# Kernel optimization log

Measured on AMD Instinct MI355X. Metric: run time of the kernel, lower is better.

Reference implementation:

```python
import jax, jax.numpy as jnp
import numpy as np
import math

B, L, H, U = 4, 4096, 1024, 1024


def setup_inputs() -> dict:
    key = jax.random.key(0)
    k_in, k_wi, k_bi, k_wo, k_bo, k_u = jax.random.split(key, 6)
    inputs = jax.random.normal(k_in, (B, L, H), dtype=jnp.float32)
    # Linear layers (torch Linear: y = x @ W.T + b), scaled like torch default init
    Wi = jax.random.normal(k_wi, (U, H), dtype=jnp.float32) / math.sqrt(H)
    bi = jax.random.normal(k_bi, (U,), dtype=jnp.float32) * 0.01
    Wo = jax.random.normal(k_wo, (H, U), dtype=jnp.float32) / math.sqrt(U)
    bo = jax.random.normal(k_bo, (H,), dtype=jnp.float32) * 0.01
    # LRU-style init of nu_log / gamma_log, exactly as in the torch __init__
    r_min, r_max = 0.9, 0.999
    u = jax.random.uniform(k_u, (U,), dtype=jnp.float32)
    nu_log = jnp.log(-0.5 * jnp.log(u * (r_max ** 2 - r_min ** 2) + r_min ** 2))
    gamma_log = jnp.log(jnp.sqrt(1.0 - jnp.exp(-jnp.exp(nu_log)) ** 2))
    params_log = jnp.stack([nu_log, gamma_log])  # [2, U]
    return {"inputs": inputs, "Wi": Wi, "bi": bi, "Wo": Wo, "bo": bo,
            "params_log": params_log}


def reference(inputs, Wi, bi, Wo, bo, params_log):
    # u = i_dense(inputs): [B, L, U]
    u = jnp.einsum('blh,uh->blu', inputs, Wi) + bi
    params = jnp.exp(params_log)
    nu, gamma = params[0], params[1]  # each [U]

    log2_L = int(np.ceil(np.log2(L)))
    pad_len = 2 ** log2_L - L
    x = jnp.pad(u, ((0, 0), (0, pad_len), (0, 0))) if pad_len else u
    Lp = 2 ** log2_L

    # Log-depth doubling parallel scan: h_t = exp(-nu) * h_{t-1} + u_t
    for i in range(1, log2_L + 1):
        l = 2 ** i
        x = x.reshape(B * Lp // l, l, U)
        x1, x2 = x[:, : l // 2], x[:, l // 2:]
        pos = jnp.arange(1, l // 2 + 1, dtype=jnp.float32)  # [l/2]
        lambs = jnp.exp(-pos[:, None] * nu)                  # [l/2, U]
        x2 = x2 + lambs * x1[:, -1:]
        x = jnp.concatenate([x1, x2], axis=1).reshape(B, Lp, U)

    x = x[:, :L] * gamma
    # o_dense: [B, L, H]
    return jnp.einsum('blu,hu->blh', x, Wo) + bo
```

## Files before the change

### kernel.cpp

```cpp
#include <hip/hip_runtime.h>

#define B_DIM 4
#define L_DIM 4096
#define H_DIM 1024
#define U_DIM 1024
#define M_DIM (B_DIM * L_DIM)
#define LC 64
#define NCH (L_DIM / LC)

using f32x4  = __attribute__((ext_vector_type(4))) float;
using bf16x8 = __attribute__((ext_vector_type(8))) __bf16;
using us8    = __attribute__((ext_vector_type(8))) unsigned short;

__device__ inline unsigned short f32_to_bf16(float f) {
  unsigned int u = __float_as_uint(f);
  u += 0x7FFF + ((u >> 16) & 1);
  return (unsigned short)(u >> 16);
}
__device__ inline float bf16_to_f32(unsigned short v) {
  return __uint_as_float((unsigned int)v << 16);
}

__device__ inline void async_load16(const void* g, void* l) {
  __builtin_amdgcn_global_load_lds(
      (const __attribute__((address_space(1))) void*)g,
      (__attribute__((address_space(3))) void*)l, 16, 0, 0);
}

#define IN_ELEMS  (M_DIM * H_DIM)
#define WI_ELEMS  (U_DIM * H_DIM)
#define WO_ELEMS  (H_DIM * U_DIM)
#define CVT_TOTAL (IN_ELEMS + WI_ELEMS + WO_ELEMS)

__global__ __launch_bounds__(256) void cvt_all(
    const float* __restrict__ inp, const float* __restrict__ wi,
    const float* __restrict__ wo,
    unsigned short* __restrict__ inp_b, unsigned short* __restrict__ wi_b,
    unsigned short* __restrict__ wo_b)
{
  size_t e = ((size_t)blockIdx.x * 256 + threadIdx.x) * 8;
  if (e >= CVT_TOTAL) return;
  const float* src; unsigned short* dst; size_t off;
  if (e < IN_ELEMS)                 { src = inp; dst = inp_b; off = e; }
  else if (e < IN_ELEMS + WI_ELEMS) { src = wi;  dst = wi_b;  off = e - IN_ELEMS; }
  else                              { src = wo;  dst = wo_b;  off = e - IN_ELEMS - WI_ELEMS; }
  f32x4 a = *(const f32x4*)(src + off);
  f32x4 b = *(const f32x4*)(src + off + 4);
  us8 r;
  r[0] = f32_to_bf16(a.x); r[1] = f32_to_bf16(a.y);
  r[2] = f32_to_bf16(a.z); r[3] = f32_to_bf16(a.w);
  r[4] = f32_to_bf16(b.x); r[5] = f32_to_bf16(b.y);
  r[6] = f32_to_bf16(b.z); r[7] = f32_to_bf16(b.w);
  *(us8*)(dst + off) = r;
}

#define TM 128
#define TN 128

template <typename OUT>
__global__ __launch_bounds__(256) void gemm_bt_bias(
    const unsigned short* __restrict__ A, const unsigned short* __restrict__ Bm,
    const float* __restrict__ bias, OUT* __restrict__ C,
    int M, int N, int K)
{
  __shared__ __attribute__((aligned(16))) unsigned short sA[2][TM * 32];
  __shared__ __attribute__((aligned(16))) unsigned short sB[2][TN * 32];

  const int tid    = threadIdx.x;
  const int lane   = tid & 63;
  const int wave   = tid >> 6;
  const int wm     = wave & 1;
  const int wn     = wave >> 1;
  const int frag_m = lane & 15;
  const int frag_kb = (lane >> 4) * 16;

  const int p    = blockIdx.y * gridDim.x + blockIdx.x;
  const int xcd  = p & 7;
  const int j    = p >> 3;
  const int slab = gridDim.y >> 3;
  const int by   = xcd * slab + (j % slab);
  const int bx   = j / slab;

  const int m0 = by * TM;
  const int n0 = bx * TN;

  const char* Ab = (const char*)A;
  const char* Bb = (const char*)Bm;
  const size_t rowbytes = (size_t)K * 2;

  const int o0 = tid * 16;
  const int o1 = o0 + 4096;
  const int r0s = o0 >> 6, c0s = o0 & 63;
  const int r1s = o1 >> 6, c1s = o1 & 63;

  f32x4 acc[4][4];
  #pragma unroll
  for (int i = 0; i < 4; ++i)
    #pragma unroll
    for (int jj = 0; jj < 4; ++jj)
      acc[i][jj] = {0.f, 0.f, 0.f, 0.f};

  for (int k0 = 0; k0 < K; k0 += 64) {
    __syncthreads();
    #pragma unroll
    for (int h = 0; h < 2; ++h) {
      const size_t kb = (size_t)(k0 + h * 32) * 2;
      async_load16(Ab + (size_t)(m0 + r0s) * rowbytes + kb + c0s, (char*)sA[h] + o0);
      async_load16(Ab + (size_t)(m0 + r1s) * rowbytes + kb + c1s, (char*)sA[h] + o1);
      async_load16(Bb + (size_t)(n0 + r0s) * rowbytes + kb + c0s, (char*)sB[h] + o0);
      async_load16(Bb + (size_t)(n0 + r1s) * rowbytes + kb + c1s, (char*)sB[h] + o1);
    }
    __syncthreads();

    #pragma unroll
    for (int h = 0; h < 2; ++h) {
      bf16x8 af[4], bf[4];
      #pragma unroll
      for (int mi = 0; mi < 4; ++mi)
        af[mi] = *(const bf16x8*)((const char*)sA[h] + (wm * 64 + mi * 16 + frag_m) * 64 + frag_kb);
      #pragma unroll
      for (int ni = 0; ni < 4; ++ni)
        bf[ni] = *(const bf16x8*)((const char*)sB[h] + (wn * 64 + ni * 16 + frag_m) * 64 + frag_kb);

      #pragma unroll
      for (int mi = 0; mi < 4; ++mi)
        #pragma unroll
        for (int ni = 0; ni < 4; ++ni)
          acc[mi][ni] = __builtin_amdgcn_mfma_f32_16x16x32_bf16(af[mi], bf[ni], acc[mi][ni], 0, 0, 0);
    }
  }

  const int rr0 = (lane >> 4) * 4;
  #pragma unroll
  for (int ni = 0; ni < 4; ++ni) {
    int col  = n0 + wn * 64 + ni * 16 + frag_m;
    float bv = bias[col];
    #pragma unroll
    for (int mi = 0; mi < 4; ++mi) {
      int rowb = m0 + wm * 64 + mi * 16 + rr0;
      #pragma unroll
      for (int r = 0; r < 4; ++r) {
        float v = acc[mi][ni][r] + bv;
        if constexpr (sizeof(OUT) == 2)
          C[(size_t)(rowb + r) * N + col] = (OUT)f32_to_bf16(v);
        else
          C[(size_t)(rowb + r) * N + col] = (OUT)v;
      }
    }
  }
}

__global__ __launch_bounds__(256) void scan_carry(
    const unsigned short* __restrict__ u, const float* __restrict__ params_log,
    float* __restrict__ carry)
{
  int uu = blockIdx.x * 256 + threadIdx.x;
  int c  = blockIdx.y;
  int b  = blockIdx.z;
  float l = expf(-expf(params_log[uu]));
  const unsigned short* p = u + (size_t)(b * L_DIM + c * LC) * U_DIM + uu;
  float s = 0.f;
  #pragma unroll 8
  for (int j = 0; j < LC; ++j)
    s = fmaf(s, l, bf16_to_f32(p[(size_t)j * U_DIM]));
  carry[((size_t)b * NCH + c) * U_DIM + uu] = s;
}

__global__ __launch_bounds__(256) void scan_prefix(
    const float* __restrict__ carry, const float* __restrict__ params_log,
    float* __restrict__ prefix)
{
  int t  = blockIdx.x * 256 + threadIdx.x;
  int b  = t >> 10;
  int uu = t & (U_DIM - 1);
  float lp = expf(-expf(params_log[uu]) * (float)LC);
  const float* cp = carry  + (size_t)b * NCH * U_DIM + uu;
  float*       pp = prefix + (size_t)b * NCH * U_DIM + uu;
  float vals[NCH];
  #pragma unroll
  for (int c = 0; c < NCH; ++c)
    vals[c] = cp[(size_t)c * U_DIM];
  float s = 0.f;
  #pragma unroll
  for (int c = 0; c < NCH; ++c) {
    pp[(size_t)c * U_DIM] = s;
    s = fmaf(s, lp, vals[c]);
  }
}

__global__ __launch_bounds__(256) void scan_apply(
    const unsigned short* __restrict__ u, const float* __restrict__ params_log,
    const float* __restrict__ prefix, unsigned short* __restrict__ x_b)
{
  int uu = blockIdx.x * 256 + threadIdx.x;
  int c  = blockIdx.y;
  int b  = blockIdx.z;
  float l = expf(-expf(params_log[uu]));
  float g = expf(params_log[U_DIM + uu]);
  float s = prefix[((size_t)b * NCH + c) * U_DIM + uu];
  const unsigned short* p = u + (size_t)(b * L_DIM + c * LC) * U_DIM + uu;
  unsigned short* q = x_b + (size_t)(b * L_DIM + c * LC) * U_DIM + uu;
  #pragma unroll 8
  for (int j = 0; j < LC; ++j) {
    s = fmaf(s, l, bf16_to_f32(p[(size_t)j * U_DIM]));
    q[(size_t)j * U_DIM] = f32_to_bf16(s * g);
  }
}

extern "C" void kernel_launch(void* const* d_in, const int* in_sizes, int n_in,
                              void* d_out, int out_size, void* d_ws, size_t ws_size,
                              hipStream_t stream)
{
  const float* inputs     = (const float*)d_in[0];
  const float* Wi         = (const float*)d_in[1];
  const float* bi         = (const float*)d_in[2];
  const float* Wo         = (const float*)d_in[3];
  const float* bo         = (const float*)d_in[4];
  const float* params_log = (const float*)d_in[5];
  float* out = (float*)d_out;

  char* ws = (char*)d_ws;
  unsigned short* u_b    = (unsigned short*)(ws);
  unsigned short* x_b    = (unsigned short*)(ws + (32u << 20));
  unsigned short* in_b   = (unsigned short*)(ws + (64u << 20));
  unsigned short* wi_b   = (unsigned short*)(ws + (96u << 20));
  unsigned short* wo_b   = (unsigned short*)(ws + (98u << 20));
  float*          carry  = (float*)(ws + (100u << 20));
  float*          prefix = (float*)(ws + (101u << 20));

  cvt_all<<<dim3((CVT_TOTAL / 8 + 255) / 256), 256, 0, stream>>>(
      inputs, Wi, Wo, in_b, wi_b, wo_b);

  gemm_bt_bias<unsigned short><<<dim3(U_DIM / TN, M_DIM / TM), 256, 0, stream>>>(
      in_b, wi_b, bi, u_b, M_DIM, U_DIM, H_DIM);

  scan_carry <<<dim3(U_DIM / 256, NCH, B_DIM), 256, 0, stream>>>(u_b, params_log, carry);
  scan_prefix<<<dim3(B_DIM * U_DIM / 256),     256, 0, stream>>>(carry, params_log, prefix);
  scan_apply <<<dim3(U_DIM / 256, NCH, B_DIM), 256, 0, stream>>>(u_b, params_log, prefix, x_b);

  gemm_bt_bias<float><<<dim3(H_DIM / TN, M_DIM / TM), 256, 0, stream>>>(
      x_b, wo_b, bo, out, M_DIM, H_DIM, U_DIM);
}
```

Before: 252.2 us.

## Software-pipeline GEMM K loop with double buffering and fuse scan prefix into fixup

Measured after the change: 263.5 us. 4.5% more time.

```diff
diff --git a/kernel.cpp b/kernel.cpp
--- a/kernel.cpp
+++ b/kernel.cpp
@@ -56,6 +56,7 @@
 
 #define TM 128
 #define TN 128
+#define BK 32
 
 template <typename OUT>
 __global__ __launch_bounds__(256) void gemm_bt_bias(
@@ -63,8 +64,8 @@
     const float* __restrict__ bias, OUT* __restrict__ C,
     int M, int N, int K)
 {
-  __shared__ __attribute__((aligned(16))) unsigned short sA[2][TM * 32];
-  __shared__ __attribute__((aligned(16))) unsigned short sB[2][TN * 32];
+  __shared__ __attribute__((aligned(16))) unsigned short sA[2][TM * BK];
+  __shared__ __attribute__((aligned(16))) unsigned short sB[2][TN * BK];
 
   const int tid    = threadIdx.x;
   const int lane   = tid & 63;
@@ -100,34 +101,41 @@
     for (int jj = 0; jj < 4; ++jj)
       acc[i][jj] = {0.f, 0.f, 0.f, 0.f};
 
-  for (int k0 = 0; k0 < K; k0 += 64) {
-    __syncthreads();
-    #pragma unroll
-    for (int h = 0; h < 2; ++h) {
-      const size_t kb = (size_t)(k0 + h * 32) * 2;
-      async_load16(Ab + (size_t)(m0 + r0s) * rowbytes + kb + c0s, (char*)sA[h] + o0);
-      async_load16(Ab + (size_t)(m0 + r1s) * rowbytes + kb + c1s, (char*)sA[h] + o1);
-      async_load16(Bb + (size_t)(n0 + r0s) * rowbytes + kb + c0s, (char*)sB[h] + o0);
-      async_load16(Bb + (size_t)(n0 + r1s) * rowbytes + kb + c1s, (char*)sB[h] + o1);
+  auto stage = [&](int s, int kk) {
+    const size_t kb = (size_t)kk * 2;
+    async_load16(Ab + (size_t)(m0 + r0s) * rowbytes + kb + c0s, (char*)sA[s] + o0);
+    async_load16(Ab + (size_t)(m0 + r1s) * rowbytes + kb + c1s, (char*)sA[s] + o1);
+    async_load16(Bb + (size_t)(n0 + r0s) * rowbytes + kb + c0s, (char*)sB[s] + o0);
+    async_load16(Bb + (size_t)(n0 + r1s) * rowbytes + kb + c1s, (char*)sB[s] + o1);
+  };
+
+  const int NI = K / BK;
+  stage(0, 0);
+
+  for (int i = 0; i < NI; ++i) {
+    if (i + 1 < NI) {
+      stage((i + 1) & 1, (i + 1) * BK);
+      asm volatile("s_waitcnt vmcnt(4)\n\ts_barrier" ::: "memory");
+    } else {
+      asm volatile("s_waitcnt vmcnt(0)\n\ts_barrier" ::: "memory");
     }
-    __syncthreads();
-
-    #pragma unroll
-    for (int h = 0; h < 2; ++h) {
-      bf16x8 af[4], bf[4];
-      #pragma unroll
-      for (int mi = 0; mi < 4; ++mi)
-        af[mi] = *(const bf16x8*)((const char*)sA[h] + (wm * 64 + mi * 16 + frag_m) * 64 + frag_kb);
+
+    const int s = i & 1;
+    bf16x8 af[4], bf[4];
+    #pragma unroll
+    for (int mi = 0; mi < 4; ++mi)
+      af[mi] = *(const bf16x8*)((const char*)sA[s] + (wm * 64 + mi * 16 + frag_m) * 64 + frag_kb);
+    #pragma unroll
+    for (int ni = 0; ni < 4; ++ni)
+      bf[ni] = *(const bf16x8*)((const char*)sB[s] + (wn * 64 + ni * 16 + frag_m) * 64 + frag_kb);
+
+    #pragma unroll
+    for (int mi = 0; mi < 4; ++mi)
       #pragma unroll
       for (int ni = 0; ni < 4; ++ni)
-        bf[ni] = *(const bf16x8*)((const char*)sB[h] + (wn * 64 + ni * 16 + frag_m) * 64 + frag_kb);
-
-      #pragma unroll
-      for (int mi = 0; mi < 4; ++mi)
-        #pragma unroll
-        for (int ni = 0; ni < 4; ++ni)
-          acc[mi][ni] = __builtin_amdgcn_mfma_f32_16x16x32_bf16(af[mi], bf[ni], acc[mi][ni], 0, 0, 0);
-    }
+        acc[mi][ni] = __builtin_amdgcn_mfma_f32_16x16x32_bf16(af[mi], bf[ni], acc[mi][ni], 0, 0, 0);
+
+    asm volatile("s_barrier" ::: "memory");
   }
 
   const int rr0 = (lane >> 4) * 4;
@@ -166,38 +174,23 @@
   carry[((size_t)b * NCH + c) * U_DIM + uu] = s;
 }
 
-__global__ __launch_bounds__(256) void scan_prefix(
-    const float* __restrict__ carry, const float* __restrict__ params_log,
-    float* __restrict__ prefix)
-{
-  int t  = blockIdx.x * 256 + threadIdx.x;
-  int b  = t >> 10;
-  int uu = t & (U_DIM - 1);
-  float lp = expf(-expf(params_log[uu]) * (float)LC);
-  const float* cp = carry  + (size_t)b * NCH * U_DIM + uu;
-  float*       pp = prefix + (size_t)b * NCH * U_DIM + uu;
-  float vals[NCH];
-  #pragma unroll
-  for (int c = 0; c < NCH; ++c)
-    vals[c] = cp[(size_t)c * U_DIM];
-  float s = 0.f;
-  #pragma unroll
-  for (int c = 0; c < NCH; ++c) {
-    pp[(size_t)c * U_DIM] = s;
-    s = fmaf(s, lp, vals[c]);
-  }
-}
-
-__global__ __launch_bounds__(256) void scan_apply(
+__global__ __launch_bounds__(256) void scan_fixup(
     const unsigned short* __restrict__ u, const float* __restrict__ params_log,
-    const float* __restrict__ prefix, unsigned short* __restrict__ x_b)
+    const float* __restrict__ carry, unsigned short* __restrict__ x_b)
 {
   int uu = blockIdx.x * 256 + threadIdx.x;
   int c  = blockIdx.y;
   int b  = blockIdx.z;
-  float l = expf(-expf(params_log[uu]));
-  float g = expf(params_log[U_DIM + uu]);
-  float s = prefix[((size_t)b * NCH + c) * U_DIM + uu];
+  float nu = expf(params_log[uu]);
+  float l  = expf(-nu);
+  float g  = expf(params_log[U_DIM + uu]);
+  float lp = expf(-nu * (float)LC);
+
+  const float* cp = carry + (size_t)b * NCH * U_DIM + uu;
+  float s = 0.f;
+  for (int cc = 0; cc < c; ++cc)
+    s = fmaf(s, lp, cp[(size_t)cc * U_DIM]);
+
   const unsigned short* p = u + (size_t)(b * L_DIM + c * LC) * U_DIM + uu;
   unsigned short* q = x_b + (size_t)(b * L_DIM + c * LC) * U_DIM + uu;
   #pragma unroll 8
@@ -226,7 +219,6 @@
   unsigned short* wi_b   = (unsigned short*)(ws + (96u << 20));
   unsigned short* wo_b   = (unsigned short*)(ws + (98u << 20));
   float*          carry  = (float*)(ws + (100u << 20));
-  float*          prefix = (float*)(ws + (101u << 20));
 
   cvt_all<<<dim3((CVT_TOTAL / 8 + 255) / 256), 256, 0, stream>>>(
       inputs, Wi, Wo, in_b, wi_b, wo_b);
@@ -234,9 +226,8 @@
   gemm_bt_bias<unsigned short><<<dim3(U_DIM / TN, M_DIM / TM), 256, 0, stream>>>(
       in_b, wi_b, bi, u_b, M_DIM, U_DIM, H_DIM);
 
-  scan_carry <<<dim3(U_DIM / 256, NCH, B_DIM), 256, 0, stream>>>(u_b, params_log, carry);
-  scan_prefix<<<dim3(B_DIM * U_DIM / 256),     256, 0, stream>>>(carry, params_log, prefix);
-  scan_apply <<<dim3(U_DIM / 256, NCH, B_DIM), 256, 0, stream>>>(u_b, params_log, prefix, x_b);
+  scan_carry<<<dim3(U_DIM / 256, NCH, B_DIM), 256, 0, stream>>>(u_b, params_log, carry);
+  scan_fixup<<<dim3(U_DIM / 256, NCH, B_DIM), 256, 0, stream>>>(u_b, params_log, carry, x_b);
 
   gemm_bt_bias<float><<<dim3(H_DIM / TN, M_DIM / TM), 256, 0, stream>>>(
       x_b, wo_b, bo, out, M_DIM, H_DIM, U_DIM);
```

## Fuse scan chunk carry into first GEMM epilogue and double-buffer GEMM loads

Applied to the files above, without the earlier changes.

Result: no change. 253.6 us (+0.5%).

```diff
diff --git a/kernel.cpp b/kernel.cpp
--- a/kernel.cpp
+++ b/kernel.cpp
@@ -56,15 +56,17 @@
 
 #define TM 128
 #define TN 128
-
-template <typename OUT>
+#define BK 32
+
+template <typename OUT, bool CARRY, int K>
 __global__ __launch_bounds__(256) void gemm_bt_bias(
     const unsigned short* __restrict__ A, const unsigned short* __restrict__ Bm,
     const float* __restrict__ bias, OUT* __restrict__ C,
-    int M, int N, int K)
-{
-  __shared__ __attribute__((aligned(16))) unsigned short sA[2][TM * 32];
-  __shared__ __attribute__((aligned(16))) unsigned short sB[2][TN * 32];
+    int M, int N,
+    float* __restrict__ carry_out, const float* __restrict__ params_log)
+{
+  __shared__ __attribute__((aligned(16))) unsigned short sA[2][TM * BK];
+  __shared__ __attribute__((aligned(16))) unsigned short sB[2][TN * BK];
 
   const int tid    = threadIdx.x;
   const int lane   = tid & 63;
@@ -72,7 +74,8 @@
   const int wm     = wave & 1;
   const int wn     = wave >> 1;
   const int frag_m = lane & 15;
-  const int frag_kb = (lane >> 4) * 16;
+  const int quad   = lane >> 4;
+  const int frag_kb = 16 * (quad ^ ((lane >> 1) & 3));
 
   const int p    = blockIdx.y * gridDim.x + blockIdx.x;
   const int xcd  = p & 7;
@@ -88,10 +91,11 @@
   const char* Bb = (const char*)Bm;
   const size_t rowbytes = (size_t)K * 2;
 
-  const int o0 = tid * 16;
-  const int o1 = o0 + 4096;
-  const int r0s = o0 >> 6, c0s = o0 & 63;
-  const int r1s = o1 >> 6, c1s = o1 & 63;
+  const int r0s  = tid >> 2;
+  const int r1s  = r0s + 64;
+  const int csw  = 16 * ((tid & 3) ^ ((tid >> 3) & 3));
+  const int o0   = tid * 16;
+  const int o1   = o0 + 4096;
 
   f32x4 acc[4][4];
   #pragma unroll
@@ -100,37 +104,45 @@
     for (int jj = 0; jj < 4; ++jj)
       acc[i][jj] = {0.f, 0.f, 0.f, 0.f};
 
-  for (int k0 = 0; k0 < K; k0 += 64) {
-    __syncthreads();
-    #pragma unroll
-    for (int h = 0; h < 2; ++h) {
-      const size_t kb = (size_t)(k0 + h * 32) * 2;
-      async_load16(Ab + (size_t)(m0 + r0s) * rowbytes + kb + c0s, (char*)sA[h] + o0);
-      async_load16(Ab + (size_t)(m0 + r1s) * rowbytes + kb + c1s, (char*)sA[h] + o1);
-      async_load16(Bb + (size_t)(n0 + r0s) * rowbytes + kb + c0s, (char*)sB[h] + o0);
-      async_load16(Bb + (size_t)(n0 + r1s) * rowbytes + kb + c1s, (char*)sB[h] + o1);
+  auto stage = [&](int s, int kk) {
+    const size_t kb = (size_t)kk * 2;
+    async_load16(Ab + (size_t)(m0 + r0s) * rowbytes + kb + csw, (char*)sA[s] + o0);
+    async_load16(Ab + (size_t)(m0 + r1s) * rowbytes + kb + csw, (char*)sA[s] + o1);
+    async_load16(Bb + (size_t)(n0 + r0s) * rowbytes + kb + csw, (char*)sB[s] + o0);
+    async_load16(Bb + (size_t)(n0 + r1s) * rowbytes + kb + csw, (char*)sB[s] + o1);
+  };
+
+  constexpr int NI = K / BK;
+  stage(0, 0);
+
+  #pragma unroll 2
+  for (int i = 0; i < NI; ++i) {
+    if (i + 1 < NI) {
+      stage((i + 1) & 1, (i + 1) * BK);
+      asm volatile("s_waitcnt vmcnt(4)\n\ts_barrier" ::: "memory");
+    } else {
+      asm volatile("s_waitcnt vmcnt(0)\n\ts_barrier" ::: "memory");
     }
-    __syncthreads();
-
-    #pragma unroll
-    for (int h = 0; h < 2; ++h) {
-      bf16x8 af[4], bf[4];
-      #pragma unroll
-      for (int mi = 0; mi < 4; ++mi)
-        af[mi] = *(const bf16x8*)((const char*)sA[h] + (wm * 64 + mi * 16 + frag_m) * 64 + frag_kb);
+
+    const int s = i & 1;
+    bf16x8 af[4], bf[4];
+    #pragma unroll
+    for (int mi = 0; mi < 4; ++mi)
+      af[mi] = *(const bf16x8*)((const char*)sA[s] + (wm * 64 + mi * 16 + frag_m) * 64 + frag_kb);
+    #pragma unroll
+    for (int ni = 0; ni < 4; ++ni)
+      bf[ni] = *(const bf16x8*)((const char*)sB[s] + (wn * 64 + ni * 16 + frag_m) * 64 + frag_kb);
+
+    #pragma unroll
+    for (int mi = 0; mi < 4; ++mi)
       #pragma unroll
       for (int ni = 0; ni < 4; ++ni)
-        bf[ni] = *(const bf16x8*)((const char*)sB[h] + (wn * 64 + ni * 16 + frag_m) * 64 + frag_kb);
-
-      #pragma unroll
-      for (int mi = 0; mi < 4; ++mi)
-        #pragma unroll
-        for (int ni = 0; ni < 4; ++ni)
-          acc[mi][ni] = __builtin_amdgcn_mfma_f32_16x16x32_bf16(af[mi], bf[ni], acc[mi][ni], 0, 0, 0);
-    }
-  }
-
-  const int rr0 = (lane >> 4) * 4;
+        acc[mi][ni] = __builtin_amdgcn_mfma_f32_16x16x32_bf16(af[mi], bf[ni], acc[mi][ni], 0, 0, 0);
+
+    asm volatile("s_barrier" ::: "memory");
+  }
+
+  const int rr0 = quad * 4;
   #pragma unroll
   for (int ni = 0; ni < 4; ++ni) {
     int col  = n0 + wn * 64 + ni * 16 + frag_m;
@@ -148,22 +160,35 @@
       }
     }
   }
-}
-
-__global__ __launch_bounds__(256) void scan_carry(
-    const unsigned short* __restrict__ u, const float* __restrict__ params_log,
-    float* __restrict__ carry)
-{
-  int uu = blockIdx.x * 256 + threadIdx.x;
-  int c  = blockIdx.y;
-  int b  = blockIdx.z;
-  float l = expf(-expf(params_log[uu]));
-  const unsigned short* p = u + (size_t)(b * L_DIM + c * LC) * U_DIM + uu;
-  float s = 0.f;
-  #pragma unroll 8
-  for (int j = 0; j < LC; ++j)
-    s = fmaf(s, l, bf16_to_f32(p[(size_t)j * U_DIM]));
-  carry[((size_t)b * NCH + c) * U_DIM + uu] = s;
+
+  if constexpr (CARRY) {
+    const int chunk = (m0 >> 6) + wm;
+    #pragma unroll
+    for (int ni = 0; ni < 4; ++ni) {
+      int col  = n0 + wn * 64 + ni * 16 + frag_m;
+      float bv = bias[col];
+      float nu = expf(params_log[col]);
+      float w_base = expf(-nu * (float)(63 - quad * 4));
+      float linv   = expf(nu);
+      float l16inv = expf(16.f * nu);
+      float part = 0.f;
+      float wmi  = w_base;
+      #pragma unroll
+      for (int mi = 0; mi < 4; ++mi) {
+        float w = wmi;
+        #pragma unroll
+        for (int r = 0; r < 4; ++r) {
+          part = fmaf(w, acc[mi][ni][r] + bv, part);
+          w *= linv;
+        }
+        wmi *= l16inv;
+      }
+      part += __shfl_xor(part, 16);
+      part += __shfl_xor(part, 32);
+      if (quad == 0)
+        carry_out[(size_t)chunk * U_DIM + col] = part;
+    }
+  }
 }
 
 __global__ __launch_bounds__(256) void scan_prefix(
@@ -231,13 +256,14 @@
   cvt_all<<<dim3((CVT_TOTAL / 8 + 255) / 256), 256, 0, stream>>>(
       inputs, Wi, Wo, in_b, wi_b, wo_b);
 
-  gemm_bt_bias<unsigned short><<<dim3(U_DIM / TN, M_DIM / TM), 256, 0, stream>>>(
-      in_b, wi_b, bi, u_b, M_DIM, U_DIM, H_DIM);
-
-  scan_carry <<<dim3(U_DIM / 256, NCH, B_DIM), 256, 0, stream>>>(u_b, params_log, carry);
+  gemm_bt_bias<unsigned short, true, H_DIM>
+      <<<dim3(U_DIM / TN, M_DIM / TM), 256, 0, stream>>>(
+      in_b, wi_b, bi, u_b, M_DIM, U_DIM, carry, params_log);
+
   scan_prefix<<<dim3(B_DIM * U_DIM / 256),     256, 0, stream>>>(carry, params_log, prefix);
   scan_apply <<<dim3(U_DIM / 256, NCH, B_DIM), 256, 0, stream>>>(u_b, params_log, prefix, x_b);
 
-  gemm_bt_bias<float><<<dim3(H_DIM / TN, M_DIM / TM), 256, 0, stream>>>(
-      x_b, wo_b, bo, out, M_DIM, H_DIM, U_DIM);
-}
+  gemm_bt_bias<float, false, U_DIM>
+      <<<dim3(H_DIM / TN, M_DIM / TM), 256, 0, stream>>>(
+      x_b, wo_b, bo, out, M_DIM, H_DIM, nullptr, nullptr);
+}
```
